# Kernel optimization log

Hardware: AMD Instinct MI355X
Metric: run time of the kernel (lower is better)

Reference implementation:

```python
import jax, jax.numpy as jnp
import numpy as np

B, N, E, D = 8, 2048, 4096, 256
HOPS = 3

def setup_inputs() -> dict:
    key = jax.random.key(0)
    ks = jax.random.split(key, 12)
    p = lambda k, shp: (jax.random.normal(k, shp, dtype=jnp.float32) * 0.02)
    return {
        "node_vec": jax.random.normal(ks[0], (B, N, D), dtype=jnp.float32),
        "edge_vec": jax.random.normal(ks[1], (B, E, D), dtype=jnp.float32),
        "node2edge": jax.random.uniform(ks[2], (B, E, N), dtype=jnp.float32),
        "edge2node": jax.random.uniform(ks[3], (B, N, E), dtype=jnp.float32),
        "node_mask": jnp.ones((B, N), dtype=jnp.float32),
        "W_fuse": p(ks[4], (D, 2 * D)), "b_fuse": jnp.zeros((D,), jnp.float32),
        "W_z": p(ks[5], (D, 4 * D)), "b_z": jnp.zeros((D,), jnp.float32),
        "W_update": p(ks[6], (D, 2 * D)),
        "W_reset": p(ks[7], (D, 2 * D)),
        "W_memory": p(ks[8], (D, 2 * D)),
        "W_max": p(ks[9], (D, D)),
    }

def _gnn_step(node_vec, edge_vec, n2e, e2n, W_fuse, b_fuse):
    # n2e: [B,E,N], e2n: [B,N,E]
    edge_emb = jnp.einsum('ben,bnd->bed', n2e, node_vec)          # [B,E,D]
    edge_emb = jax.nn.relu(jnp.concatenate([edge_emb, edge_vec], axis=-1) @ W_fuse.T + b_fuse)
    norm = jnp.sum(e2n, axis=2, keepdims=True) + 1.0               # [B,N,1]
    return (jnp.einsum('bne,bed->bnd', e2n, edge_emb) + node_vec) / norm

def _gated_fusion(in_vec, out_vec, W_z, b_z):
    feats = jnp.concatenate([in_vec, out_vec, in_vec * out_vec, in_vec - out_vec], axis=-1)
    z = jax.nn.sigmoid(feats @ W_z.T + b_z)
    return (1.0 - z) * in_vec + z * out_vec

def _gru_step(cur, new, W_u, W_r, W_m):
    cn = jnp.concatenate([cur, new], axis=-1)
    u = jax.nn.sigmoid(cn @ W_u.T)
    r = jax.nn.sigmoid(cn @ W_r.T)
    m = jnp.tanh(jnp.concatenate([r * cur, new], axis=-1) @ W_m.T)
    return (1.0 - u) * cur + u * m

def reference(node_vec, edge_vec, node2edge, edge2node, node_mask,
              W_fuse, b_fuse, W_z, b_z, W_update, W_reset, W_memory, W_max):
    n2e_T = jnp.swapaxes(node2edge, 1, 2)  # [B,N,E]
    e2n_T = jnp.swapaxes(edge2node, 1, 2)  # [B,E,N]
    for _ in range(HOPS):
        out_vec = _gnn_step(node_vec, edge_vec, node2edge, edge2node, W_fuse, b_fuse)
        in_vec = _gnn_step(node_vec, edge_vec, e2n_T, n2e_T, W_fuse, b_fuse)
        new_vec = _gated_fusion(in_vec, out_vec, W_z, b_z)
        node_vec = _gru_step(node_vec, new_vec, W_update, W_reset, W_memory)
    # graph max-pooling: linear then max over nodes (node_mask unused, as in original)
    graph_embedding = jnp.max(node_vec @ W_max.T, axis=1)          # [B,D]
    return (jnp.swapaxes(node_vec, 0, 1), graph_embedding[None])    # [N,B,D], [1,B,D]
```

## Files before the change

### kernel.cpp

```cpp
#include <hip/hip_runtime.h>
#include <math.h>

#define Bb 8
#define Nn 2048
#define Ee 4096
#define Dd 256
#define HOPS 3

typedef __attribute__((ext_vector_type(4))) float f32x4;
typedef _Float16 f16;
typedef __attribute__((ext_vector_type(8))) _Float16 f16x8;
typedef __attribute__((ext_vector_type(4))) _Float16 f16x4;
typedef __attribute__((ext_vector_type(8))) short s16x8;
typedef __attribute__((ext_vector_type(4))) short s16x4;

__device__ __forceinline__ short f2bf(float f){
  union{float f; unsigned u;} x; x.f=f;
  unsigned r = (x.u + 0x7fffu + ((x.u>>16)&1u)) >> 16;
  return (short)r;
}
__device__ __forceinline__ float bf2f(short h){
  union{unsigned u; float f;} x; x.u = ((unsigned)(unsigned short)h) << 16; return x.f;
}
__device__ __forceinline__ int swz(int row, int idx){ return idx ^ ((row & 7) << 3); }

enum { HN=0, HT=1 };
enum { OF=0, OH=1, OHT=2 };
enum { EP_NONE=0, EP_BIAS, EP_ADDRELU, EP_AGG };
enum { SM_CN=0, SM_G4, SM_RC };
enum { SE_GATE=0, SE_SIG, SE_TANH };

template<int AMODE, bool AH, int SPL, int EPI, int OUTM>
__global__ __launch_bounds__(512) void hgemm(
    const void* __restrict__ Av, const f16* __restrict__ Bh, void* __restrict__ Cv,
    const float* __restrict__ aux1, const float* __restrict__ aux2,
    const float* __restrict__ bias,
    int M, int Nd, int K, int lda, int ldb, int ldc,
    long sA, long sB, long sC, long sAux1, long sAux2,
    long aLo, long bLo, int maskB, int mask1)
{
  const int bz = blockIdx.z;
  const char* Ab = (const char*)Av + (AH ? bz * sA * 2 : bz * sA * 4);
  Bh += (long)(bz & maskB) * sB;
  char* Cb = (char*)Cv + ((OUTM == OF) ? bz * sC * 4 : bz * sC * 2);
  if (aux1) aux1 += (long)(bz & mask1) * sAux1;
  if (aux2) aux2 += bz * sAux2;
  const int m0 = blockIdx.y * 128;
  const int n0 = blockIdx.x * 128;

  constexpr int HLA = 128 * 64;
  constexpr int HLB = 128 * 64;
  __shared__ f16 As[128 * 64 * ((SPL & 2) ? 2 : 1)];
  __shared__ f16 Bs[128 * 64 * ((SPL & 1) ? 2 : 1)];

  const int tid = threadIdx.x;
  const int wid = tid >> 6, lane = tid & 63;
  const int wm = (wid >> 1) * 32, wn = (wid & 1) * 64;
  const int r = lane & 15, g = lane >> 4;

  f32x4 acc[2][4];
  #pragma unroll
  for (int i = 0; i < 2; i++)
    #pragma unroll
    for (int j = 0; j < 4; j++) acc[i][j] = (f32x4){0.f, 0.f, 0.f, 0.f};

  f16x8 ra0, ra1, rl0, rl1;
  f16x8 rb0, rb1, rbl0, rbl1;

  auto loadA = [&](int k0) {
    if (AMODE == HN && AH) {
      const f16* Ah = (const f16*)Ab;
      const int row = tid >> 2, kc = (tid & 3) * 16;
      const long off = (long)(m0 + row) * lda + k0 + kc;
      ra0 = *(const f16x8*)&Ah[off];
      ra1 = *(const f16x8*)&Ah[off + 8];
      if (SPL & 2) { rl0 = *(const f16x8*)&Ah[aLo + off]; rl1 = *(const f16x8*)&Ah[aLo + off + 8]; }
    } else if (AMODE == HN && !AH) {
      const float* Af = (const float*)Ab;
      const int row = tid >> 2, kc = (tid & 3) * 16;
      const float* s = &Af[(long)(m0 + row) * lda + k0 + kc];
      f32x4 v0 = *(const f32x4*)s,       v1 = *(const f32x4*)(s + 4);
      f32x4 v2 = *(const f32x4*)(s + 8), v3 = *(const f32x4*)(s + 12);
      ra0 = (f16x8){(f16)v0.x,(f16)v0.y,(f16)v0.z,(f16)v0.w,(f16)v1.x,(f16)v1.y,(f16)v1.z,(f16)v1.w};
      ra1 = (f16x8){(f16)v2.x,(f16)v2.y,(f16)v2.z,(f16)v2.w,(f16)v3.x,(f16)v3.y,(f16)v3.z,(f16)v3.w};
    } else {
      const int mm = tid & 127, kh = (tid >> 7) * 16;
      if (AH) {
        const f16* s = &((const f16*)Ab)[(long)(k0 + kh) * lda + m0 + mm];
        #pragma unroll
        for (int j = 0; j < 8; j++) ra0[j] = s[(long)j * lda];
        #pragma unroll
        for (int j = 0; j < 8; j++) ra1[j] = s[(long)(j + 8) * lda];
      } else {
        const float* s = &((const float*)Ab)[(long)(k0 + kh) * lda + m0 + mm];
        #pragma unroll
        for (int j = 0; j < 8; j++) ra0[j] = (f16)s[(long)j * lda];
        #pragma unroll
        for (int j = 0; j < 8; j++) ra1[j] = (f16)s[(long)(j + 8) * lda];
      }
    }
  };
  auto storeA = [&]() {
    if (AMODE == HT) {
      const int mm = tid & 127, kh = (tid >> 7) * 16;
      *(f16x8*)&As[swz(mm, mm * 64 + kh)]     = ra0;
      *(f16x8*)&As[swz(mm, mm * 64 + kh + 8)] = ra1;
    } else {
      const int row = tid >> 2, kc = (tid & 3) * 16;
      const int i0 = swz(row, row * 64 + kc), i1 = swz(row, row * 64 + kc + 8);
      *(f16x8*)&As[i0] = ra0;
      *(f16x8*)&As[i1] = ra1;
      if (SPL & 2) { *(f16x8*)&As[HLA + i0] = rl0; *(f16x8*)&As[HLA + i1] = rl1; }
    }
  };
  auto loadB = [&](int k0) {
    const int row = tid >> 2, kc = (tid & 3) * 16;
    const long off = (long)(n0 + row) * ldb + k0 + kc;
    rb0 = *(const f16x8*)&Bh[off];
    rb1 = *(const f16x8*)&Bh[off + 8];
    if (SPL & 1) { rbl0 = *(const f16x8*)&Bh[bLo + off]; rbl1 = *(const f16x8*)&Bh[bLo + off + 8]; }
  };
  auto storeB = [&]() {
    const int row = tid >> 2, kc = (tid & 3) * 16;
    const int i0 = swz(row, row * 64 + kc), i1 = swz(row, row * 64 + kc + 8);
    *(f16x8*)&Bs[i0] = rb0;
    *(f16x8*)&Bs[i1] = rb1;
    if (SPL & 1) { *(f16x8*)&Bs[HLB + i0] = rbl0; *(f16x8*)&Bs[HLB + i1] = rbl1; }
  };

  loadA(0); loadB(0);
  storeA(); storeB();
  __syncthreads();

  const int NT = K >> 6;
  for (int t = 0; t < NT; t++) {
    const bool more = (t + 1 < NT);
    if (more) { loadA((t + 1) << 6); loadB((t + 1) << 6); }
    #pragma unroll
    for (int ks = 0; ks < 2; ks++) {
      f16x8 af[2], bf[4], afl[2], bfl[4];
      #pragma unroll
      for (int i = 0; i < 2; i++) {
        const int rw = wm + i * 16 + r;
        const int ix = swz(rw, rw * 64 + ks * 32 + g * 8);
        af[i] = *(const f16x8*)&As[ix];
        if (SPL & 2) afl[i] = *(const f16x8*)&As[HLA + ix];
      }
      #pragma unroll
      for (int j = 0; j < 4; j++) {
        const int rw = wn + j * 16 + r;
        const int ix = swz(rw, rw * 64 + ks * 32 + g * 8);
        bf[j] = *(const f16x8*)&Bs[ix];
        if (SPL & 1) bfl[j] = *(const f16x8*)&Bs[HLB + ix];
      }
      #pragma unroll
      for (int i = 0; i < 2; i++)
        #pragma unroll
        for (int j = 0; j < 4; j++) {
          acc[i][j] = __builtin_amdgcn_mfma_f32_16x16x32_f16(af[i], bf[j], acc[i][j], 0, 0, 0);
          if (SPL & 1)
            acc[i][j] = __builtin_amdgcn_mfma_f32_16x16x32_f16(af[i], bfl[j], acc[i][j], 0, 0, 0);
          if (SPL & 2)
            acc[i][j] = __builtin_amdgcn_mfma_f32_16x16x32_f16(afl[i], bf[j], acc[i][j], 0, 0, 0);
        }
    }
    __syncthreads();
    if (more) { storeA(); storeB(); __syncthreads(); }
  }

  if (OUTM == OHT) {
    f16* tile = (f16*)Bs;
    #pragma unroll
    for (int half = 0; half < 2; half++) {
      __syncthreads();
      if ((wm >> 6) == half) {
        #pragma unroll
        for (int i = 0; i < 2; i++)
          #pragma unroll
          for (int j = 0; j < 4; j++) {
            const int rowl = wm + i * 16 + g * 4 - 64 * half;
            const int coll = wn + j * 16 + r;
            #pragma unroll
            for (int t = 0; t < 4; t++) {
              float v = acc[i][j][t];
              if (EPI == EP_ADDRELU) {
                v += aux1[(long)(m0 + 64 * half + rowl + t) * 256 + n0 + coll];
                v = v > 0.f ? v : 0.f;
              } else if (EPI == EP_BIAS) { v += bias[n0 + coll]; }
              tile[coll * 72 + rowl + t] = (f16)v;
            }
          }
      }
      __syncthreads();
      const int c2 = tid >> 2, rs = (tid & 3) * 16;
      f16* dst = &((f16*)Cb)[(long)(n0 + c2) * ldc + m0 + 64 * half + rs];
      *(f16x8*)dst       = *(const f16x8*)&tile[c2 * 72 + rs];
      *(f16x8*)(dst + 8) = *(const f16x8*)&tile[c2 * 72 + rs + 8];
    }
  } else {
    #pragma unroll
    for (int i = 0; i < 2; i++) {
      #pragma unroll
      for (int j = 0; j < 4; j++) {
        const int rowb = m0 + wm + i * 16 + g * 4;
        const int col = n0 + wn + j * 16 + r;
        #pragma unroll
        for (int t = 0; t < 4; t++) {
          const int row = rowb + t;
          const long idx = (long)row * ldc + col;
          float v = acc[i][j][t];
          if (EPI == EP_BIAS)         { v += bias[col]; }
          else if (EPI == EP_ADDRELU) { v += aux1[(long)row * 256 + col]; v = v > 0.f ? v : 0.f; }
          else if (EPI == EP_AGG)     { v = (v + aux1[idx]) * aux2[row]; }
          if (OUTM == OH) ((f16*)Cb)[idx] = (f16)v;
          else            ((float*)Cb)[idx] = v;
        }
      }
    }
  }
}

template<int AMODE, int EPI>
__global__ __launch_bounds__(512) void ggemm(
    const float* __restrict__ A, const float* __restrict__ A2, const float* __restrict__ A3,
    const short* __restrict__ Bw, float* __restrict__ C,
    const float* __restrict__ aux1, const float* __restrict__ aux2, const float* __restrict__ bias,
    int Nd, int K, int lda, int ldb, int ldc, long bLo)
{
  const int m0 = blockIdx.y * 128;
  const int n0 = blockIdx.x * 128;
  constexpr int HLA = 128 * 64;
  constexpr int HLB = 128 * 64;
  __shared__ short As[128 * 64 * 2];
  __shared__ short Bs[128 * 64 * 2];

  const int tid = threadIdx.x;
  const int wid = tid >> 6, lane = tid & 63;
  const int wm = (wid >> 1) * 32, wn = (wid & 1) * 64;
  const int r = lane & 15, g = lane >> 4;

  f32x4 acc[2][4];
  #pragma unroll
  for (int i = 0; i < 2; i++)
    #pragma unroll
    for (int j = 0; j < 4; j++) acc[i][j] = (f32x4){0.f, 0.f, 0.f, 0.f};

  s16x4 rah[4], ral[4];
  s16x8 rbh0, rbh1, rbl0, rbl1;

  auto loadA = [&](int k0) {
    const int row = tid >> 2, kc = (tid & 3) * 16;
    const int kk = k0 + kc, q = kk >> 8, kd = kk & 255;
    const long base = (long)(m0 + row) * 256 + kd;
    const long baseA = (long)(m0 + row) * lda + kd;
    #pragma unroll
    for (int u = 0; u < 4; u++) {
      f32x4 v;
      if (AMODE == SM_CN) {
        v = (q == 0) ? *(const f32x4*)(A + base + 4 * u)
                     : *(const f32x4*)(A2 + base + 4 * u);
      } else if (AMODE == SM_G4) {
        if (q == 0)      v = *(const f32x4*)(A  + base + 4 * u);
        else if (q == 1) v = *(const f32x4*)(A2 + base + 4 * u);
        else {
          f32x4 x = *(const f32x4*)(A  + base + 4 * u);
          f32x4 y = *(const f32x4*)(A2 + base + 4 * u);
          v = (q == 2) ? x * y : x - y;
        }
      } else {
        if (q == 0) {
          f32x4 x = *(const f32x4*)(A  + baseA + 4 * u);
          f32x4 y = *(const f32x4*)(A2 + base + 4 * u);
          v = x * y;
        } else v = *(const f32x4*)(A3 + base + 4 * u);
      }
      s16x4 h = { f2bf(v.x), f2bf(v.y), f2bf(v.z), f2bf(v.w) };
      rah[u] = h;
      ral[u] = (s16x4){ f2bf(v.x - bf2f(h.x)), f2bf(v.y - bf2f(h.y)),
                        f2bf(v.z - bf2f(h.z)), f2bf(v.w - bf2f(h.w)) };
    }
  };
  auto storeA = [&]() {
    const int row = tid >> 2, kc = (tid & 3) * 16;
    const int i0 = swz(row, row * 64 + kc), i1 = swz(row, row * 64 + kc + 8);
    *(s16x4*)&As[i0]     = rah[0]; *(s16x4*)&As[i0 + 4] = rah[1];
    *(s16x4*)&As[i1]     = rah[2]; *(s16x4*)&As[i1 + 4] = rah[3];
    *(s16x4*)&As[HLA + i0]     = ral[0]; *(s16x4*)&As[HLA + i0 + 4] = ral[1];
    *(s16x4*)&As[HLA + i1]     = ral[2]; *(s16x4*)&As[HLA + i1 + 4] = ral[3];
  };
  auto loadB = [&](int k0) {
    const int row = tid >> 2, kc = (tid & 3) * 16;
    const long off = (long)(n0 + row) * ldb + k0 + kc;
    rbh0 = *(const s16x8*)&Bw[off];
    rbh1 = *(const s16x8*)&Bw[off + 8];
    rbl0 = *(const s16x8*)&Bw[bLo + off];
    rbl1 = *(const s16x8*)&Bw[bLo + off + 8];
  };
  auto storeB = [&]() {
    const int row = tid >> 2, kc = (tid & 3) * 16;
    const int i0 = swz(row, row * 64 + kc), i1 = swz(row, row * 64 + kc + 8);
    *(s16x8*)&Bs[i0] = rbh0;
    *(s16x8*)&Bs[i1] = rbh1;
    *(s16x8*)&Bs[HLB + i0] = rbl0;
    *(s16x8*)&Bs[HLB + i1] = rbl1;
  };

  loadA(0); loadB(0);
  storeA(); storeB();
  __syncthreads();

  const int NT = K >> 6;
  for (int t = 0; t < NT; t++) {
    const bool more = (t + 1 < NT);
    if (more) { loadA((t + 1) << 6); loadB((t + 1) << 6); }
    #pragma unroll
    for (int ks = 0; ks < 2; ks++) {
      s16x8 ah[2], al[2], bh[4], bl[4];
      #pragma unroll
      for (int i = 0; i < 2; i++) {
        const int rw = wm + i * 16 + r;
        const int ix = swz(rw, rw * 64 + ks * 32 + g * 8);
        ah[i] = *(const s16x8*)&As[ix];
        al[i] = *(const s16x8*)&As[HLA + ix];
      }
      #pragma unroll
      for (int j = 0; j < 4; j++) {
        const int rw = wn + j * 16 + r;
        const int ix = swz(rw, rw * 64 + ks * 32 + g * 8);
        bh[j] = *(const s16x8*)&Bs[ix];
        bl[j] = *(const s16x8*)&Bs[HLB + ix];
      }
      #pragma unroll
      for (int i = 0; i < 2; i++)
        #pragma unroll
        for (int j = 0; j < 4; j++) {
          acc[i][j] = __builtin_amdgcn_mfma_f32_16x16x32_bf16(ah[i], bh[j], acc[i][j], 0, 0, 0);
          acc[i][j] = __builtin_amdgcn_mfma_f32_16x16x32_bf16(ah[i], bl[j], acc[i][j], 0, 0, 0);
          acc[i][j] = __builtin_amdgcn_mfma_f32_16x16x32_bf16(al[i], bh[j], acc[i][j], 0, 0, 0);
        }
    }
    __syncthreads();
    if (more) { storeA(); storeB(); __syncthreads(); }
  }

  #pragma unroll
  for (int i = 0; i < 2; i++) {
    #pragma unroll
    for (int j = 0; j < 4; j++) {
      #pragma unroll
      for (int t = 0; t < 4; t++) {
        const int row = m0 + wm + i * 16 + g * 4 + t;
        const int col = n0 + wn + j * 16 + r;
        float v = acc[i][j][t];
        if (EPI == SE_GATE) {
          v += bias[col];
          float z = 1.f / (1.f + __expf(-v));
          const long ix = (long)row * 256 + col;
          v = (1.f - z) * aux1[ix] + z * aux2[ix];
        } else if (EPI == SE_SIG) {
          v = 1.f / (1.f + __expf(-v));
        } else {
          v = tanhf(v);
        }
        C[(long)row * ldc + col] = v;
      }
    }
  }
}


__global__ void cvt_n2e_colsum(const float* __restrict__ n2e, f16* __restrict__ n2e_h,
                               float* __restrict__ part) {
  const int n = blockIdx.x * 256 + threadIdx.x;
  const int c = blockIdx.y, b = blockIdx.z;
  const long base = (long)b * Ee * Nn + (long)c * 256 * Nn + n;
  float s = 0.f;
  for (int e = 0; e < 256; e++) {
    float v = n2e[base + (long)e * Nn];
    n2e_h[base + (long)e * Nn] = (f16)v;
    s += v;
  }
  part[((long)b * 16 + c) * Nn + n] = s;
}

__global__ void cvt_e2n_rowsum(const float* __restrict__ e2n, f16* __restrict__ e2n_h,
                               float* __restrict__ rno) {
  const long row = blockIdx.x;
  const int tid = threadIdx.x, lane = tid & 63, wid = tid >> 6;
  const float* p = e2n + row * Ee;
  f16* ph = e2n_h + row * Ee;
  float s = 0.f;
  for (int e = tid; e < Ee; e += 256) { float v = p[e]; ph[e] = (f16)v; s += v; }
  #pragma unroll
  for (int off = 32; off; off >>= 1) s += __shfl_down(s, off);
  __shared__ float wsum[4];
  if (lane == 0) wsum[wid] = s;
  __syncthreads();
  if (tid == 0) rno[row] = 1.f / (1.f + wsum[0] + wsum[1] + wsum[2] + wsum[3]);
}

__global__ void adjT(const f16* __restrict__ in, f16* __restrict__ out, int R, int C) {
  __shared__ f16 t[64][72];
  const long boff = (long)blockIdx.z * R * C;
  const int r0 = blockIdx.x * 64, c0 = blockIdx.y * 64;
  const int tid = threadIdx.x;
  const int rl = tid >> 2, cl = (tid & 3) * 16;
  const f16* src = in + boff + (long)(r0 + rl) * C + c0 + cl;
  *(f16x8*)&t[rl][cl]     = *(const f16x8*)src;
  *(f16x8*)&t[rl][cl + 8] = *(const f16x8*)(src + 8);
  __syncthreads();
  const int cl2 = tid >> 2, rl2 = (tid & 3) * 16;
  f16x8 o0, o1;
  #pragma unroll
  for (int v = 0; v < 8; v++) { o0[v] = t[rl2 + v][cl2]; o1[v] = t[rl2 + 8 + v][cl2]; }
  f16* dst = out + boff + (long)(c0 + cl2) * R + r0 + rl2;
  *(f16x8*)dst = o0;
  *(f16x8*)(dst + 8) = o1;
}

__global__ void rowsum_kernel(const float* __restrict__ e2n, float* __restrict__ out) {
  const int gw = blockIdx.x * 4 + (threadIdx.x >> 6);
  const int lane = threadIdx.x & 63;
  const float* p = e2n + (long)gw * Ee;
  float s = 0.f;
  for (int e = lane; e < Ee; e += 64) s += p[e];
  #pragma unroll
  for (int off = 32; off; off >>= 1) s += __shfl_down(s, off);
  if (lane == 0) out[gw] = 1.f / (1.f + s);
}
__global__ void colsum_kernel(const float* __restrict__ n2e, float* __restrict__ part) {
  const int n = blockIdx.x * 256 + threadIdx.x;
  const int c = blockIdx.y, b = blockIdx.z;
  const float* p = n2e + (long)b * Ee * Nn + (long)c * 256 * Nn + n;
  float s = 0.f;
  for (int e = 0; e < 256; e++) s += p[(long)e * Nn];
  part[((long)b * 16 + c) * Nn + n] = s;
}
__global__ void colfin_kernel(const float* __restrict__ part, float* __restrict__ rni) {
  const int i = blockIdx.x * 256 + threadIdx.x;
  const int b = i >> 11, n = i & 2047;
  float s = 0.f;
  #pragma unroll
  for (int c = 0; c < 16; c++) s += part[((long)b * 16 + c) * Nn + n];
  rni[i] = 1.f / (1.f + s);
}

__global__ void cvt_half(const float* __restrict__ src, f16* __restrict__ dst) {
  const long i4 = (long)blockIdx.x * 256 + threadIdx.x;
  f32x4 v = *(const f32x4*)&src[i4 * 4];
  *(f16x4*)&dst[i4 * 4] = (f16x4){(f16)v.x, (f16)v.y, (f16)v.z, (f16)v.w};
}

__global__ void cvt_half_split(const float* __restrict__ src, f16* __restrict__ dst, long loOff) {
  const long i4 = (long)blockIdx.x * 256 + threadIdx.x;
  f32x4 v = *(const f32x4*)&src[i4 * 4];
  f16x4 h = {(f16)v.x, (f16)v.y, (f16)v.z, (f16)v.w};
  *(f16x4*)&dst[i4 * 4] = h;
  f16x4 l = {(f16)(v.x - (float)h[0]), (f16)(v.y - (float)h[1]),
             (f16)(v.z - (float)h[2]), (f16)(v.w - (float)h[3])};
  *(f16x4*)&dst[loOff + i4 * 4] = l;
}

__global__ void cvt_bf_split(const float* __restrict__ src, short* __restrict__ dst, long loOff) {
  const long i4 = (long)blockIdx.x * 256 + threadIdx.x;
  f32x4 v = *(const f32x4*)&src[i4 * 4];
  s16x4 h = { f2bf(v.x), f2bf(v.y), f2bf(v.z), f2bf(v.w) };
  *(s16x4*)&dst[i4 * 4] = h;
  s16x4 l = { f2bf(v.x - bf2f(h.x)), f2bf(v.y - bf2f(h.y)),
              f2bf(v.z - bf2f(h.z)), f2bf(v.w - bf2f(h.w)) };
  *(s16x4*)&dst[loOff + i4 * 4] = l;
}

__global__ void init_cur(const float* __restrict__ node_vec, float* __restrict__ cur,
                         f16* __restrict__ cur_h, long loOff) {
  const long i4 = (long)blockIdx.x * 256 + threadIdx.x;
  f32x4 v = *(const f32x4*)&node_vec[i4 * 4];
  *(f32x4*)&cur[i4 * 4] = v;
  f16x4 h = {(f16)v.x, (f16)v.y, (f16)v.z, (f16)v.w};
  *(f16x4*)&cur_h[i4 * 4] = h;
  f16x4 l = {(f16)(v.x - (float)h[0]), (f16)(v.y - (float)h[1]),
             (f16)(v.z - (float)h[2]), (f16)(v.w - (float)h[3])};
  *(f16x4*)&cur_h[loOff + i4 * 4] = l;
}

__global__ void transposeT(const float* __restrict__ cur, f16* __restrict__ curT, long loOff) {
  __shared__ f16 th[64][72];
  __shared__ f16 tl[64][72];
  const int b = blockIdx.z, nt = blockIdx.x * 64, dt = blockIdx.y * 64;
  const int tid = threadIdx.x;
  const int nl = tid >> 2, d0 = (tid & 3) * 16;
  const float* src = cur + ((long)b * Nn + nt + nl) * 256 + dt + d0;
  #pragma unroll
  for (int u = 0; u < 4; u++) {
    f32x4 v = *(const f32x4*)(src + 4 * u);
    f16x4 h = {(f16)v.x, (f16)v.y, (f16)v.z, (f16)v.w};
    *(f16x4*)&th[nl][d0 + 4 * u] = h;
    f16x4 l = {(f16)(v.x - (float)h[0]), (f16)(v.y - (float)h[1]),
               (f16)(v.z - (float)h[2]), (f16)(v.w - (float)h[3])};
    *(f16x4*)&tl[nl][d0 + 4 * u] = l;
  }
  __syncthreads();
  const int dl = tid >> 2, n0l = (tid & 3) * 16;
  f16x8 o0, o1, p0, p1;
  #pragma unroll
  for (int v = 0; v < 8; v++) {
    o0[v] = th[n0l + v][dl];     o1[v] = th[n0l + 8 + v][dl];
    p0[v] = tl[n0l + v][dl];     p1[v] = tl[n0l + 8 + v][dl];
  }
  f16* dst = curT + (long)b * (256 * Nn) + (long)(dt + dl) * Nn + nt + n0l;
  *(f16x8*)dst = o0;
  *(f16x8*)(dst + 8) = o1;
  *(f16x8*)(dst + loOff) = p0;
  *(f16x8*)(dst + loOff + 8) = p1;
}

__global__ void gruf_kernel(const float* __restrict__ urb, const float* __restrict__ m,
                            float* __restrict__ cur, f16* __restrict__ cur_h, long loOff) {
  const long i = (long)blockIdx.x * 256 + threadIdx.x;
  const long bn = i >> 8; const int d = i & 255;
  const float uu = urb[bn * 512 + d];
  const float v = (1.f - uu) * cur[i] + uu * m[i];
  cur[i] = v;
  f16 h = (f16)v;
  cur_h[i] = h;
  cur_h[loOff + i] = (f16)(v - (float)h);
}

__global__ void maxpool1(const float* __restrict__ pooled, float* __restrict__ part) {
  const int d = threadIdx.x, c = blockIdx.x, b = blockIdx.y;
  const float* p = pooled + ((long)b * Nn + c * 256) * Dd + d;
  float m = -INFINITY;
  for (int n = 0; n < 256; n++) m = fmaxf(m, p[(long)n * Dd]);
  part[(b * 8 + c) * Dd + d] = m;
}
__global__ void maxpool2(const float* __restrict__ part, float* __restrict__ out1) {
  const int d = threadIdx.x, b = blockIdx.x;
  float m = -INFINITY;
  #pragma unroll
  for (int c = 0; c < 8; c++) m = fmaxf(m, part[(b * 8 + c) * Dd + d]);
  out1[b * Dd + d] = m;
}
__global__ void transpose_out(const float* __restrict__ cur, float* __restrict__ out0) {
  const long i = (long)blockIdx.x * 256 + threadIdx.x;
  const int d = i & 255;
  const long nb = i >> 8;
  const int b = nb & 7;
  const long n = nb >> 3;
  out0[i] = cur[((long)b * Nn + n) * Dd + d];
}

extern "C" void kernel_launch(void* const* d_in, const int* in_sizes, int n_in,
                              void* d_out, int out_size, void* d_ws, size_t ws_size,
                              hipStream_t stream) {
  const float* node_vec = (const float*)d_in[0];
  const float* edge_vec = (const float*)d_in[1];
  const float* n2e      = (const float*)d_in[2];
  const float* e2n      = (const float*)d_in[3];
  const float* W_fuse   = (const float*)d_in[5];
  const float* b_fuse   = (const float*)d_in[6];
  const float* W_z      = (const float*)d_in[7];
  const float* b_z      = (const float*)d_in[8];
  const float* W_u      = (const float*)d_in[9];
  const float* W_r      = (const float*)d_in[10];
  const float* W_m      = (const float*)d_in[11];
  const float* W_max    = (const float*)d_in[12];

  const long ND  = (long)Bb * Nn * Dd;
  const long EDb = (long)Ee * Dd;
  const long NDb = (long)Nn * Dd;
  const long ED  = (long)Bb * EDb;
  const long ADJb = (long)Ee * Nn;
  const long ADJ = (long)Bb * ADJb;
  const int  BN  = Bb * Nn;

  char* p = (char*)d_ws;
  auto alloc = [&](size_t bytes) { char* r = p; p += (bytes + 255) & ~(size_t)255; return r; };

  const size_t need_full =
      (size_t)4 * ADJ * 2
      + (size_t)ED * 2
      + (size_t)4 * ED * 2
      + (size_t)ED * 4
      + (size_t)4 * ND * 2
      + (size_t)(2 * 131072 + 2 * 65536) * 2
      + (size_t)(2 * 262144 + 2 * 262144 + 2 * 131072) * 2
      + (size_t)5 * ND * 4
      + (size_t)BN * 512 * 4
      + (size_t)(2 * BN + 16 * BN + BN) * 4
      + 64 * 1024;
  const bool full = ws_size >= need_full;

  f16 *adjEO = nullptr, *adjAG = nullptr;
  f16 *n2e_h = nullptr, *e2n_hT = nullptr, *e2n_h = nullptr, *n2e_hT = nullptr;
  if (full) {
    adjEO = (f16*)alloc((size_t)2 * ADJ * 2);
    adjAG = (f16*)alloc((size_t)2 * ADJ * 2);
    n2e_h = adjEO;  e2n_hT = adjEO + ADJ;
    e2n_h = adjAG;  n2e_hT = adjAG + ADJ;
  }
  f16* ev_h    = (f16*)alloc(ED * 2);
  f16* E1h2    = (f16*)alloc((size_t)2 * ED * 2);
  f16* E2T2    = (f16*)alloc((size_t)2 * ED * 2);
  float* EVW   = (float*)alloc(ED * 4);
  f16* cur_h   = (f16*)alloc(2 * ND * 2);
  f16* cur_hT  = (f16*)alloc(2 * ND * 2);
  f16* Wf_h    = (f16*)alloc(2 * 131072 * 2);
  f16* Wmax_h  = (f16*)alloc(2 * 65536 * 2);
  short* Wz_s  = (short*)alloc((size_t)2 * 262144 * 2);
  short* Wur_s = (short*)alloc((size_t)2 * 262144 * 2);
  short* Wm_s  = (short*)alloc((size_t)2 * 131072 * 2);
  float* cur   = (float*)alloc(ND * 4);
  float* outv  = (float*)alloc(2 * ND * 4);
  float* inv   = outv + ND;
  float* nv    = (float*)alloc(ND * 4);
  float* urb   = (float*)alloc((size_t)BN * 512 * 4);
  float* mb    = (float*)alloc(ND * 4);
  float* rno   = (float*)alloc(2 * BN * 4);
  float* rni   = rno + BN;
  float* colpart = (float*)alloc((size_t)16 * BN * 4);
  float* maxpart = (float*)alloc(BN * 4);

  float* out0 = (float*)d_out;
  float* out1 = out0 + ND;

  if (full) {
    cvt_n2e_colsum<<<dim3(Nn / 256, 16, Bb), 256, 0, stream>>>(n2e, n2e_h, colpart);
    colfin_kernel<<<BN / 256, 256, 0, stream>>>(colpart, rni);
    cvt_e2n_rowsum<<<BN, 256, 0, stream>>>(e2n, e2n_h, rno);
    adjT<<<dim3(Ee / 64, Nn / 64, Bb), 256, 0, stream>>>(n2e_h, n2e_hT, Ee, Nn);
    adjT<<<dim3(Nn / 64, Ee / 64, Bb), 256, 0, stream>>>(e2n_h, e2n_hT, Nn, Ee);
  } else {
    colsum_kernel<<<dim3(Nn / 256, 16, Bb), 256, 0, stream>>>(n2e, colpart);
    colfin_kernel<<<BN / 256, 256, 0, stream>>>(colpart, rni);
    rowsum_kernel<<<BN / 4, 256, 0, stream>>>(e2n, rno);
  }
  cvt_half<<<(int)(ED / 1024), 256, 0, stream>>>(edge_vec, ev_h);
  cvt_half_split<<<131072 / 1024, 256, 0, stream>>>(W_fuse, Wf_h, 131072);
  cvt_half_split<<<65536 / 1024, 256, 0, stream>>>(W_max, Wmax_h, 65536);
  cvt_bf_split<<<262144 / 1024, 256, 0, stream>>>(W_z, Wz_s, 262144);
  cvt_bf_split<<<131072 / 1024, 256, 0, stream>>>(W_u, Wur_s, 262144);
  cvt_bf_split<<<131072 / 1024, 256, 0, stream>>>(W_r, Wur_s + 131072, 262144);
  cvt_bf_split<<<131072 / 1024, 256, 0, stream>>>(W_m, Wm_s, 131072);
  init_cur<<<(int)(ND / 1024), 256, 0, stream>>>(node_vec, cur, cur_h, ND);
  transposeT<<<dim3(Nn / 64, 4, Bb), 256, 0, stream>>>(cur, cur_hT, ND);

  hgemm<HN, true, 1, EP_BIAS, OF><<<dim3(2, Ee / 128, Bb), 512, 0, stream>>>(
      ev_h, Wf_h + 256, EVW, nullptr, nullptr, b_fuse,
      Ee, 256, 256, 256, 512, 256, EDb, 0, EDb, 0, 0, 0, 131072, 0, 0);

  for (int h = 0; h < HOPS; h++) {
    if (full) {
      hgemm<HN, true, 1, EP_NONE, OH><<<dim3(2, Ee / 128, 2 * Bb), 512, 0, stream>>>(
          adjEO, cur_hT, E1h2, nullptr, nullptr, nullptr,
          Ee, 256, Nn, Nn, Nn, 256, ADJb, NDb, EDb, 0, 0, 0, ND, 7, 0);
      hgemm<HN, true, 1, EP_ADDRELU, OHT><<<dim3(2, Ee / 128, 2 * Bb), 512, 0, stream>>>(
          E1h2, Wf_h, E2T2, EVW, nullptr, nullptr,
          Ee, 256, 256, 256, 512, Ee, EDb, 0, EDb, EDb, 0, 0, 131072, 0, 7);
      hgemm<HN, true, 0, EP_AGG, OF><<<dim3(2, Nn / 128, 2 * Bb), 512, 0, stream>>>(
          adjAG, E2T2, outv, cur, rno, nullptr,
          Nn, 256, Ee, Ee, Ee, 256, ADJb, EDb, NDb, NDb, (long)Nn, 0, 0, 15, 7);
    } else {
      hgemm<HN, false, 1, EP_NONE, OH><<<dim3(2, Ee / 128, Bb), 512, 0, stream>>>(
          n2e, cur_hT, E1h2, nullptr, nullptr, nullptr,
          Ee, 256, Nn, Nn, Nn, 256, ADJb, NDb, EDb, 0, 0, 0, ND, 7, 0);
      hgemm<HT, false, 1, EP_NONE, OH><<<dim3(2, Ee / 128, Bb), 512, 0, stream>>>(
          e2n, cur_hT, E1h2 + ED, nullptr, nullptr, nullptr,
          Ee, 256, Nn, Ee, Nn, 256, ADJb, NDb, EDb, 0, 0, 0, ND, 7, 0);
      hgemm<HN, true, 1, EP_ADDRELU, OHT><<<dim3(2, Ee / 128, 2 * Bb), 512, 0, stream>>>(
          E1h2, Wf_h, E2T2, EVW, nullptr, nullptr,
          Ee, 256, 256, 256, 512, Ee, EDb, 0, EDb, EDb, 0, 0, 131072, 0, 7);
      hgemm<HN, false, 0, EP_AGG, OF><<<dim3(2, Nn / 128, Bb), 512, 0, stream>>>(
          e2n, E2T2, outv, cur, rno, nullptr,
          Nn, 256, Ee, Ee, Ee, 256, (long)Nn * Ee, EDb, NDb, NDb, (long)Nn, 0, 0, 15, 7);
      hgemm<HT, false, 0, EP_AGG, OF><<<dim3(2, Nn / 128, Bb), 512, 0, stream>>>(
          n2e, E2T2 + ED, inv, cur, rni, nullptr,
          Nn, 256, Ee, Nn, Ee, 256, (long)Ee * Nn, EDb, NDb, NDb, (long)Nn, 0, 0, 15, 7);
    }
    ggemm<SM_G4, SE_GATE><<<dim3(2, BN / 128, 1), 512, 0, stream>>>(
        inv, outv, nullptr, Wz_s, nv, inv, outv, b_z, 256, 1024, 256, 1024, 256, 262144);
    ggemm<SM_CN, SE_SIG><<<dim3(4, BN / 128, 1), 512, 0, stream>>>(
        cur, nv, nullptr, Wur_s, urb, nullptr, nullptr, nullptr, 512, 512, 256, 512, 512, 262144);
    ggemm<SM_RC, SE_TANH><<<dim3(2, BN / 128, 1), 512, 0, stream>>>(
        urb + 256, cur, nv, Wm_s, mb, nullptr, nullptr, nullptr, 256, 512, 512, 512, 256, 131072);
    gruf_kernel<<<(int)(ND / 256), 256, 0, stream>>>(urb, mb, cur, cur_h, ND);
    if (h < HOPS - 1)
      transposeT<<<dim3(Nn / 64, 4, Bb), 256, 0, stream>>>(cur, cur_hT, ND);
  }

  hgemm<HN, true, 3, EP_NONE, OF><<<dim3(2, BN / 128, 1), 512, 0, stream>>>(
      cur_h, Wmax_h, urb, nullptr, nullptr, nullptr,
      BN, 256, 256, 256, 256, 256, 0, 0, 0, 0, 0, ND, 65536, 0, 0);
  maxpool1<<<dim3(8, Bb), 256, 0, stream>>>(urb, maxpart);
  maxpool2<<<Bb, 256, 0, stream>>>(maxpart, out1);

  transpose_out<<<(int)(ND / 256), 256, 0, stream>>>(cur, out0);
}
```

Before: 1.709 ms.

## Switch GEMMs to 32x32 MFMA, fuse adjacency convert/transpose/sums, store EVW in fp16

Both GEMM kernels drop the 16x16x32 MFMA tiling in favour of 32x32x16 MFMA, with two 16-register accumulators per wave, and the epilogue index maps are rewritten to match. The separate adjacency conversion, row/column-sum and transpose kernels are merged into one cvt_dual kernel that reads each fp32 adjacency once and writes both the fp16 copy and its transpose, plus partial sums that a small kernel then reduces. The edge_vec@W_fuse bias term is stored in fp16 instead of fp32, halving its traffic in the add-relu epilogue but adding rounding error. The larger MFMA shape cuts LDS fragment loads per FLOP and the fused preprocessing removes extra passes over the large adjacency matrices.

```diff
diff --git a/kernel.cpp b/kernel.cpp
--- a/kernel.cpp
+++ b/kernel.cpp
@@ -8,6 +8,7 @@
 #define HOPS 3
 
 typedef __attribute__((ext_vector_type(4))) float f32x4;
+typedef __attribute__((ext_vector_type(16))) float f32x16;
 typedef _Float16 f16;
 typedef __attribute__((ext_vector_type(8))) _Float16 f16x8;
 typedef __attribute__((ext_vector_type(4))) _Float16 f16x4;
@@ -26,7 +27,7 @@
 
 enum { HN=0, HT=1 };
 enum { OF=0, OH=1, OHT=2 };
-enum { EP_NONE=0, EP_BIAS, EP_ADDRELU, EP_AGG };
+enum { EP_NONE=0, EP_BIAS, EP_ADDRELUH, EP_AGG };
 enum { SM_CN=0, SM_G4, SM_RC };
 enum { SE_GATE=0, SE_SIG, SE_TANH };
 
@@ -56,13 +57,9 @@
   const int tid = threadIdx.x;
   const int wid = tid >> 6, lane = tid & 63;
   const int wm = (wid >> 1) * 32, wn = (wid & 1) * 64;
-  const int r = lane & 15, g = lane >> 4;
-
-  f32x4 acc[2][4];
-  #pragma unroll
-  for (int i = 0; i < 2; i++)
-    #pragma unroll
-    for (int j = 0; j < 4; j++) acc[i][j] = (f32x4){0.f, 0.f, 0.f, 0.f};
+  const int l31 = lane & 31, lh = lane >> 5;
+
+  f32x16 acc0 = {0.f}, acc1 = {0.f};
 
   f16x8 ra0, ra1, rl0, rl1;
   f16x8 rb0, rb1, rbl0, rbl1;
@@ -137,32 +134,32 @@
     const bool more = (t + 1 < NT);
     if (more) { loadA((t + 1) << 6); loadB((t + 1) << 6); }
     #pragma unroll
-    for (int ks = 0; ks < 2; ks++) {
-      f16x8 af[2], bf[4], afl[2], bfl[4];
-      #pragma unroll
-      for (int i = 0; i < 2; i++) {
-        const int rw = wm + i * 16 + r;
-        const int ix = swz(rw, rw * 64 + ks * 32 + g * 8);
-        af[i] = *(const f16x8*)&As[ix];
-        if (SPL & 2) afl[i] = *(const f16x8*)&As[HLA + ix];
-      }
-      #pragma unroll
-      for (int j = 0; j < 4; j++) {
-        const int rw = wn + j * 16 + r;
-        const int ix = swz(rw, rw * 64 + ks * 32 + g * 8);
-        bf[j] = *(const f16x8*)&Bs[ix];
-        if (SPL & 1) bfl[j] = *(const f16x8*)&Bs[HLB + ix];
-      }
-      #pragma unroll
-      for (int i = 0; i < 2; i++)
-        #pragma unroll
-        for (int j = 0; j < 4; j++) {
-          acc[i][j] = __builtin_amdgcn_mfma_f32_16x16x32_f16(af[i], bf[j], acc[i][j], 0, 0, 0);
-          if (SPL & 1)
-            acc[i][j] = __builtin_amdgcn_mfma_f32_16x16x32_f16(af[i], bfl[j], acc[i][j], 0, 0, 0);
-          if (SPL & 2)
-            acc[i][j] = __builtin_amdgcn_mfma_f32_16x16x32_f16(afl[i], bf[j], acc[i][j], 0, 0, 0);
-        }
+    for (int ks = 0; ks < 4; ks++) {
+      const int kb = ks * 16 + lh * 8;
+      f16x8 af, afl, bf0, bf1, bfl0, bfl1;
+      {
+        const int rw = wm + l31;
+        const int ix = swz(rw, rw * 64 + kb);
+        af = *(const f16x8*)&As[ix];
+        if (SPL & 2) afl = *(const f16x8*)&As[HLA + ix];
+      }
+      {
+        const int rw0 = wn + l31, rw1 = wn + 32 + l31;
+        const int ix0 = swz(rw0, rw0 * 64 + kb), ix1 = swz(rw1, rw1 * 64 + kb);
+        bf0 = *(const f16x8*)&Bs[ix0];
+        bf1 = *(const f16x8*)&Bs[ix1];
+        if (SPL & 1) { bfl0 = *(const f16x8*)&Bs[HLB + ix0]; bfl1 = *(const f16x8*)&Bs[HLB + ix1]; }
+      }
+      acc0 = __builtin_amdgcn_mfma_f32_32x32x16_f16(af, bf0, acc0, 0, 0, 0);
+      acc1 = __builtin_amdgcn_mfma_f32_32x32x16_f16(af, bf1, acc1, 0, 0, 0);
+      if (SPL & 1) {
+        acc0 = __builtin_amdgcn_mfma_f32_32x32x16_f16(af, bfl0, acc0, 0, 0, 0);
+        acc1 = __builtin_amdgcn_mfma_f32_32x32x16_f16(af, bfl1, acc1, 0, 0, 0);
+      }
+      if (SPL & 2) {
+        acc0 = __builtin_amdgcn_mfma_f32_32x32x16_f16(afl, bf0, acc0, 0, 0, 0);
+        acc1 = __builtin_amdgcn_mfma_f32_32x32x16_f16(afl, bf1, acc1, 0, 0, 0);
+      }
     }
     __syncthreads();
     if (more) { storeA(); storeB(); __syncthreads(); }
@@ -175,21 +172,19 @@
       __syncthreads();
       if ((wm >> 6) == half) {
         #pragma unroll
-        for (int i = 0; i < 2; i++)
+        for (int j = 0; j < 2; j++) {
+          const int coll = wn + j * 32 + l31;
           #pragma unroll
-          for (int j = 0; j < 4; j++) {
-            const int rowl = wm + i * 16 + g * 4 - 64 * half;
-            const int coll = wn + j * 16 + r;
-            #pragma unroll
-            for (int t = 0; t < 4; t++) {
-              float v = acc[i][j][t];
-              if (EPI == EP_ADDRELU) {
-                v += aux1[(long)(m0 + 64 * half + rowl + t) * 256 + n0 + coll];
-                v = v > 0.f ? v : 0.f;
-              } else if (EPI == EP_BIAS) { v += bias[n0 + coll]; }
-              tile[coll * 72 + rowl + t] = (f16)v;
-            }
+          for (int reg = 0; reg < 16; reg++) {
+            const int rowl = wm - 64 * half + (reg & 3) + 8 * (reg >> 2) + 4 * lh;
+            float v = j ? acc1[reg] : acc0[reg];
+            if (EPI == EP_ADDRELUH) {
+              v += (float)((const f16*)aux1)[(long)(m0 + 64 * half + rowl) * 256 + n0 + coll];
+              v = v > 0.f ? v : 0.f;
+            } else if (EPI == EP_BIAS) { v += bias[n0 + coll]; }
+            tile[coll * 72 + rowl] = (f16)v;
           }
+        }
       }
       __syncthreads();
       const int c2 = tid >> 2, rs = (tid & 3) * 16;
@@ -199,22 +194,19 @@
     }
   } else {
     #pragma unroll
-    for (int i = 0; i < 2; i++) {
+    for (int j = 0; j < 2; j++) {
+      const int col = n0 + wn + j * 32 + l31;
       #pragma unroll
-      for (int j = 0; j < 4; j++) {
-        const int rowb = m0 + wm + i * 16 + g * 4;
-        const int col = n0 + wn + j * 16 + r;
-        #pragma unroll
-        for (int t = 0; t < 4; t++) {
-          const int row = rowb + t;
-          const long idx = (long)row * ldc + col;
-          float v = acc[i][j][t];
-          if (EPI == EP_BIAS)         { v += bias[col]; }
-          else if (EPI == EP_ADDRELU) { v += aux1[(long)row * 256 + col]; v = v > 0.f ? v : 0.f; }
-          else if (EPI == EP_AGG)     { v = (v + aux1[idx]) * aux2[row]; }
-          if (OUTM == OH) ((f16*)Cb)[idx] = (f16)v;
-          else            ((float*)Cb)[idx] = v;
-        }
+      for (int reg = 0; reg < 16; reg++) {
+        const int row = m0 + wm + (reg & 3) + 8 * (reg >> 2) + 4 * lh;
+        const long idx = (long)row * ldc + col;
+        float v = j ? acc1[reg] : acc0[reg];
+        if (EPI == EP_BIAS)          { v += bias[col]; }
+        else if (EPI == EP_ADDRELUH) { v += (float)((const f16*)aux1)[(long)row * 256 + col];
+                                       v = v > 0.f ? v : 0.f; }
+        else if (EPI == EP_AGG)      { v = (v + aux1[idx]) * aux2[row]; }
+        if (OUTM == OH) ((f16*)Cb)[idx] = (f16)v;
+        else            ((float*)Cb)[idx] = v;
       }
     }
   }
@@ -237,13 +229,9 @@
   const int tid = threadIdx.x;
   const int wid = tid >> 6, lane = tid & 63;
   const int wm = (wid >> 1) * 32, wn = (wid & 1) * 64;
-  const int r = lane & 15, g = lane >> 4;
-
-  f32x4 acc[2][4];
-  #pragma unroll
-  for (int i = 0; i < 2; i++)
-    #pragma unroll
-    for (int j = 0; j < 4; j++) acc[i][j] = (f32x4){0.f, 0.f, 0.f, 0.f};
+  const int l31 = lane & 31, lh = lane >> 5;
+
+  f32x16 acc0 = {0.f}, acc1 = {0.f};
 
   s16x4 rah[4], ral[4];
   s16x8 rbh0, rbh1, rbl0, rbl1;
@@ -314,108 +302,110 @@
     const bool more = (t + 1 < NT);
     if (more) { loadA((t + 1) << 6); loadB((t + 1) << 6); }
     #pragma unroll
-    for (int ks = 0; ks < 2; ks++) {
-      s16x8 ah[2], al[2], bh[4], bl[4];
-      #pragma unroll
-      for (int i = 0; i < 2; i++) {
-        const int rw = wm + i * 16 + r;
-        const int ix = swz(rw, rw * 64 + ks * 32 + g * 8);
-        ah[i] = *(const s16x8*)&As[ix];
-        al[i] = *(const s16x8*)&As[HLA + ix];
-      }
-      #pragma unroll
-      for (int j = 0; j < 4; j++) {
-        const int rw = wn + j * 16 + r;
-        const int ix = swz(rw, rw * 64 + ks * 32 + g * 8);
-        bh[j] = *(const s16x8*)&Bs[ix];
-        bl[j] = *(const s16x8*)&Bs[HLB + ix];
-      }
-      #pragma unroll
-      for (int i = 0; i < 2; i++)
-        #pragma unroll
-        for (int j = 0; j < 4; j++) {
-          acc[i][j] = __builtin_amdgcn_mfma_f32_16x16x32_bf16(ah[i], bh[j], acc[i][j], 0, 0, 0);
-          acc[i][j] = __builtin_amdgcn_mfma_f32_16x16x32_bf16(ah[i], bl[j], acc[i][j], 0, 0, 0);
-          acc[i][j] = __builtin_amdgcn_mfma_f32_16x16x32_bf16(al[i], bh[j], acc[i][j], 0, 0, 0);
-        }
+    for (int ks = 0; ks < 4; ks++) {
+      const int kb = ks * 16 + lh * 8;
+      s16x8 ah, al, bh0, bh1, bl0, bl1;
+      {
+        const int rw = wm + l31;
+        const int ix = swz(rw, rw * 64 + kb);
+        ah = *(const s16x8*)&As[ix];
+        al = *(const s16x8*)&As[HLA + ix];
+      }
+      {
+        const int rw0 = wn + l31, rw1 = wn + 32 + l31;
+        const int ix0 = swz(rw0, rw0 * 64 + kb), ix1 = swz(rw1, rw1 * 64 + kb);
+        bh0 = *(const s16x8*)&Bs[ix0];
+        bh1 = *(const s16x8*)&Bs[ix1];
+        bl0 = *(const s16x8*)&Bs[HLB + ix0];
+        bl1 = *(const s16x8*)&Bs[HLB + ix1];
+      }
+      acc0 = __builtin_amdgcn_mfma_f32_32x32x16_bf16(ah, bh0, acc0, 0, 0, 0);
+      acc1 = __builtin_amdgcn_mfma_f32_32x32x16_bf16(ah, bh1, acc1, 0, 0, 0);
+      acc0 = __builtin_amdgcn_mfma_f32_32x32x16_bf16(ah, bl0, acc0, 0, 0, 0);
+      acc1 = __builtin_amdgcn_mfma_f32_32x32x16_bf16(ah, bl1, acc1, 0, 0, 0);
+      acc0 = __builtin_amdgcn_mfma_f32_32x32x16_bf16(al, bh0, acc0, 0, 0, 0);
+      acc1 = __builtin_amdgcn_mfma_f32_32x32x16_bf16(al, bh1, acc1, 0, 0, 0);
     }
     __syncthreads();
     if (more) { storeA(); storeB(); __syncthreads(); }
   }
 
   #pragma unroll
-  for (int i = 0; i < 2; i++) {
+  for (int j = 0; j < 2; j++) {
+    const int col = n0 + wn + j * 32 + l31;
     #pragma unroll
-    for (int j = 0; j < 4; j++) {
-      #pragma unroll
-      for (int t = 0; t < 4; t++) {
-        const int row = m0 + wm + i * 16 + g * 4 + t;
-        const int col = n0 + wn + j * 16 + r;
-        float v = acc[i][j][t];
-        if (EPI == SE_GATE) {
-          v += bias[col];
-          float z = 1.f / (1.f + __expf(-v));
-          const long ix = (long)row * 256 + col;
-          v = (1.f - z) * aux1[ix] + z * aux2[ix];
-        } else if (EPI == SE_SIG) {
-          v = 1.f / (1.f + __expf(-v));
-        } else {
-          v = tanhf(v);
-        }
-        C[(long)row * ldc + col] = v;
-      }
-    }
-  }
-}
-
-
-__global__ void cvt_n2e_colsum(const float* __restrict__ n2e, f16* __restrict__ n2e_h,
-                               float* __restrict__ part) {
-  const int n = blockIdx.x * 256 + threadIdx.x;
-  const int c = blockIdx.y, b = blockIdx.z;
-  const long base = (long)b * Ee * Nn + (long)c * 256 * Nn + n;
-  float s = 0.f;
-  for (int e = 0; e < 256; e++) {
-    float v = n2e[base + (long)e * Nn];
-    n2e_h[base + (long)e * Nn] = (f16)v;
-    s += v;
-  }
-  part[((long)b * 16 + c) * Nn + n] = s;
-}
-
-__global__ void cvt_e2n_rowsum(const float* __restrict__ e2n, f16* __restrict__ e2n_h,
-                               float* __restrict__ rno) {
-  const long row = blockIdx.x;
-  const int tid = threadIdx.x, lane = tid & 63, wid = tid >> 6;
-  const float* p = e2n + row * Ee;
-  f16* ph = e2n_h + row * Ee;
-  float s = 0.f;
-  for (int e = tid; e < Ee; e += 256) { float v = p[e]; ph[e] = (f16)v; s += v; }
-  #pragma unroll
-  for (int off = 32; off; off >>= 1) s += __shfl_down(s, off);
-  __shared__ float wsum[4];
-  if (lane == 0) wsum[wid] = s;
-  __syncthreads();
-  if (tid == 0) rno[row] = 1.f / (1.f + wsum[0] + wsum[1] + wsum[2] + wsum[3]);
-}
-
-__global__ void adjT(const f16* __restrict__ in, f16* __restrict__ out, int R, int C) {
+    for (int reg = 0; reg < 16; reg++) {
+      const int row = m0 + wm + (reg & 3) + 8 * (reg >> 2) + 4 * lh;
+      float v = j ? acc1[reg] : acc0[reg];
+      if (EPI == SE_GATE) {
+        v += bias[col];
+        float z = 1.f / (1.f + __expf(-v));
+        const long ix = (long)row * 256 + col;
+        v = (1.f - z) * aux1[ix] + z * aux2[ix];
+      } else if (EPI == SE_SIG) {
+        v = 1.f / (1.f + __expf(-v));
+      } else {
+        v = tanhf(v);
+      }
+      C[(long)row * ldc + col] = v;
+    }
+  }
+}
+
+
+template<bool SUMDST>
+__global__ void cvt_dual(const float* __restrict__ in, f16* __restrict__ outR,
+                         f16* __restrict__ outT, float* __restrict__ part, int R, int C) {
   __shared__ f16 t[64][72];
-  const long boff = (long)blockIdx.z * R * C;
+  __shared__ float sacc[64][4];
+  const long boff = (long)blockIdx.z * (long)R * C;
   const int r0 = blockIdx.x * 64, c0 = blockIdx.y * 64;
   const int tid = threadIdx.x;
   const int rl = tid >> 2, cl = (tid & 3) * 16;
-  const f16* src = in + boff + (long)(r0 + rl) * C + c0 + cl;
-  *(f16x8*)&t[rl][cl]     = *(const f16x8*)src;
-  *(f16x8*)&t[rl][cl + 8] = *(const f16x8*)(src + 8);
+  const float* src = in + boff + (long)(r0 + rl) * C + c0 + cl;
+  f16 loc[16];
+  float s = 0.f;
+  #pragma unroll
+  for (int u = 0; u < 4; u++) {
+    f32x4 v = *(const f32x4*)(src + 4 * u);
+    loc[4*u+0] = (f16)v.x; loc[4*u+1] = (f16)v.y; loc[4*u+2] = (f16)v.z; loc[4*u+3] = (f16)v.w;
+    if (!SUMDST) s += v.x + v.y + v.z + v.w;
+  }
+  f16* dR = outR + boff + (long)(r0 + rl) * C + c0 + cl;
+  *(f16x8*)dR       = *(const f16x8*)&loc[0];
+  *(f16x8*)(dR + 8) = *(const f16x8*)&loc[8];
+  *(f16x8*)&t[rl][cl]     = *(const f16x8*)&loc[0];
+  *(f16x8*)&t[rl][cl + 8] = *(const f16x8*)&loc[8];
+  if (!SUMDST) sacc[rl][tid & 3] = s;
   __syncthreads();
   const int cl2 = tid >> 2, rl2 = (tid & 3) * 16;
   f16x8 o0, o1;
   #pragma unroll
   for (int v = 0; v < 8; v++) { o0[v] = t[rl2 + v][cl2]; o1[v] = t[rl2 + 8 + v][cl2]; }
-  f16* dst = out + boff + (long)(c0 + cl2) * R + r0 + rl2;
-  *(f16x8*)dst = o0;
-  *(f16x8*)(dst + 8) = o1;
+  if (SUMDST) {
+    float s2 = 0.f;
+    #pragma unroll
+    for (int v = 0; v < 8; v++) s2 += (float)o0[v] + (float)o1[v];
+    sacc[cl2][tid & 3] = s2;
+  }
+  f16* dT = outT + boff + (long)(c0 + cl2) * R + r0 + rl2;
+  *(f16x8*)dT = o0;
+  *(f16x8*)(dT + 8) = o1;
+  __syncthreads();
+  if (tid < 64) {
+    float tot = sacc[tid][0] + sacc[tid][1] + sacc[tid][2] + sacc[tid][3];
+    const int slot = SUMDST ? blockIdx.x : blockIdx.y;
+    const int n    = (SUMDST ? c0 : r0) + tid;
+    part[((long)blockIdx.z * 64 + slot) * Nn + n] = tot;
+  }
+}
+
+__global__ void colfin64(const float* __restrict__ part, float* __restrict__ rn) {
+  const int i = blockIdx.x * 256 + threadIdx.x;
+  const int b = i >> 11, n = i & 2047;
+  float s = 0.f;
+  for (int c = 0; c < 64; c++) s += part[((long)b * 64 + c) * Nn + n];
+  rn[i] = 1.f / (1.f + s);
 }
 
 __global__ void rowsum_kernel(const float* __restrict__ e2n, float* __restrict__ out) {
@@ -436,7 +426,7 @@
   for (int e = 0; e < 256; e++) s += p[(long)e * Nn];
   part[((long)b * 16 + c) * Nn + n] = s;
 }
-__global__ void colfin_kernel(const float* __restrict__ part, float* __restrict__ rni) {
+__global__ void colfin16(const float* __restrict__ part, float* __restrict__ rni) {
   const int i = blockIdx.x * 256 + threadIdx.x;
   const int b = i >> 11, n = i & 2047;
   float s = 0.f;
@@ -580,13 +570,13 @@
       (size_t)4 * ADJ * 2
       + (size_t)ED * 2
       + (size_t)4 * ED * 2
-      + (size_t)ED * 4
+      + (size_t)ED * 2
       + (size_t)4 * ND * 2
       + (size_t)(2 * 131072 + 2 * 65536) * 2
       + (size_t)(2 * 262144 + 2 * 262144 + 2 * 131072) * 2
       + (size_t)5 * ND * 4
       + (size_t)BN * 512 * 4
-      + (size_t)(2 * BN + 16 * BN + BN) * 4
+      + (size_t)(2 * BN + 2 * 64 * BN) * 4
       + 64 * 1024;
   const bool full = ws_size >= need_full;
 
@@ -601,7 +591,7 @@
   f16* ev_h    = (f16*)alloc(ED * 2);
   f16* E1h2    = (f16*)alloc((size_t)2 * ED * 2);
   f16* E2T2    = (f16*)alloc((size_t)2 * ED * 2);
-  float* EVW   = (float*)alloc(ED * 4);
+  f16* EVWh    = (f16*)alloc(ED * 2);
   f16* cur_h   = (f16*)alloc(2 * ND * 2);
   f16* cur_hT  = (f16*)alloc(2 * ND * 2);
   f16* Wf_h    = (f16*)alloc(2 * 131072 * 2);
@@ -617,21 +607,23 @@
   float* mb    = (float*)alloc(ND * 4);
   float* rno   = (float*)alloc(2 * BN * 4);
   float* rni   = rno + BN;
-  float* colpart = (float*)alloc((size_t)16 * BN * 4);
+  float* rnopart = (float*)alloc((size_t)64 * BN * 4);
+  float* rnipart = (float*)alloc((size_t)64 * BN * 4);
   float* maxpart = (float*)alloc(BN * 4);
 
   float* out0 = (float*)d_out;
   float* out1 = out0 + ND;
 
   if (full) {
-    cvt_n2e_colsum<<<dim3(Nn / 256, 16, Bb), 256, 0, stream>>>(n2e, n2e_h, colpart);
-    colfin_kernel<<<BN / 256, 256, 0, stream>>>(colpart, rni);
-    cvt_e2n_rowsum<<<BN, 256, 0, stream>>>(e2n, e2n_h, rno);
-    adjT<<<dim3(Ee / 64, Nn / 64, Bb), 256, 0, stream>>>(n2e_h, n2e_hT, Ee, Nn);
-    adjT<<<dim3(Nn / 64, Ee / 64, Bb), 256, 0, stream>>>(e2n_h, e2n_hT, Nn, Ee);
+    cvt_dual<false><<<dim3(Nn / 64, Ee / 64, Bb), 256, 0, stream>>>(
+        e2n, e2n_h, e2n_hT, rnopart, Nn, Ee);
+    cvt_dual<true><<<dim3(Ee / 64, Nn / 64, Bb), 256, 0, stream>>>(
+        n2e, n2e_h, n2e_hT, rnipart, Ee, Nn);
+    colfin64<<<BN / 256, 256, 0, stream>>>(rnopart, rno);
+    colfin64<<<BN / 256, 256, 0, stream>>>(rnipart, rni);
   } else {
-    colsum_kernel<<<dim3(Nn / 256, 16, Bb), 256, 0, stream>>>(n2e, colpart);
-    colfin_kernel<<<BN / 256, 256, 0, stream>>>(colpart, rni);
+    colsum_kernel<<<dim3(Nn / 256, 16, Bb), 256, 0, stream>>>(n2e, rnipart);
+    colfin16<<<BN / 256, 256, 0, stream>>>(rnipart, rni);
     rowsum_kernel<<<BN / 4, 256, 0, stream>>>(e2n, rno);
   }
   cvt_half<<<(int)(ED / 1024), 256, 0, stream>>>(edge_vec, ev_h);
@@ -644,8 +636,8 @@
   init_cur<<<(int)(ND / 1024), 256, 0, stream>>>(node_vec, cur, cur_h, ND);
   transposeT<<<dim3(Nn / 64, 4, Bb), 256, 0, stream>>>(cur, cur_hT, ND);
 
-  hgemm<HN, true, 1, EP_BIAS, OF><<<dim3(2, Ee / 128, Bb), 512, 0, stream>>>(
-      ev_h, Wf_h + 256, EVW, nullptr, nullptr, b_fuse,
+  hgemm<HN, true, 1, EP_BIAS, OH><<<dim3(2, Ee / 128, Bb), 512, 0, stream>>>(
+      ev_h, Wf_h + 256, EVWh, nullptr, nullptr, b_fuse,
       Ee, 256, 256, 256, 512, 256, EDb, 0, EDb, 0, 0, 0, 131072, 0, 0);
 
   for (int h = 0; h < HOPS; h++) {
@@ -653,9 +645,9 @@
       hgemm<HN, true, 1, EP_NONE, OH><<<dim3(2, Ee / 128, 2 * Bb), 512, 0, stream>>>(
           adjEO, cur_hT, E1h2, nullptr, nullptr, nullptr,
           Ee, 256, Nn, Nn, Nn, 256, ADJb, NDb, EDb, 0, 0, 0, ND, 7, 0);
-      hgemm<HN, true, 1, EP_ADDRELU, OHT><<<dim3(2, Ee / 128, 2 * Bb), 512, 0, stream>>>(
-          E1h2, Wf_h, E2T2, EVW, nullptr, nullptr,
-          Ee, 256, 256, 256, 512, Ee, EDb, 0, EDb, EDb, 0, 0, 131072, 0, 7);
+      hgemm<HN, true, 1, EP_ADDRELUH, OHT><<<dim3(2, Ee / 128, 2 * Bb), 512, 0, stream>>>(
+          E1h2, Wf_h, E2T2, (const float*)EVWh, nullptr, nullptr,
+          Ee, 256, 256, 256, 512, Ee, EDb, 0, EDb, EDb / 2, 0, 0, 131072, 0, 7);
       hgemm<HN, true, 0, EP_AGG, OF><<<dim3(2, Nn / 128, 2 * Bb), 512, 0, stream>>>(
           adjAG, E2T2, outv, cur, rno, nullptr,
           Nn, 256, Ee, Ee, Ee, 256, ADJb, EDb, NDb, NDb, (long)Nn, 0, 0, 15, 7);
@@ -666,9 +658,9 @@
       hgemm<HT, false, 1, EP_NONE, OH><<<dim3(2, Ee / 128, Bb), 512, 0, stream>>>(
           e2n, cur_hT, E1h2 + ED, nullptr, nullptr, nullptr,
           Ee, 256, Nn, Ee, Nn, 256, ADJb, NDb, EDb, 0, 0, 0, ND, 7, 0);
-      hgemm<HN, true, 1, EP_ADDRELU, OHT><<<dim3(2, Ee / 128, 2 * Bb), 512, 0, stream>>>(
-          E1h2, Wf_h, E2T2, EVW, nullptr, nullptr,
-          Ee, 256, 256, 256, 512, Ee, EDb, 0, EDb, EDb, 0, 0, 131072, 0, 7);
+      hgemm<HN, true, 1, EP_ADDRELUH, OHT><<<dim3(2, Ee / 128, 2 * Bb), 512, 0, stream>>>(
+          E1h2, Wf_h, E2T2, (const float*)EVWh, nullptr, nullptr,
+          Ee, 256, 256, 256, 512, Ee, EDb, 0, EDb, EDb / 2, 0, 0, 131072, 0, 7);
       hgemm<HN, false, 0, EP_AGG, OF><<<dim3(2, Nn / 128, Bb), 512, 0, stream>>>(
           e2n, E2T2, outv, cur, rno, nullptr,
           Nn, 256, Ee, Ee, Ee, 256, (long)Nn * Ee, EDb, NDb, NDb, (long)Nn, 0, 0, 15, 7);
```

Measured after the change: 1.781 ms. 1.04x slower.
